# Performance work log

Hardware: AMD Instinct MI355X
Metric: run time of the kernel (lower is better)

Reference implementation:

```python
import jax, jax.numpy as jnp
import numpy as np

N_EMBD = 1024
N_HEAD = 16
HEAD_SIZE = N_EMBD // N_HEAD
EPS = 1e-5

def layer_norm(x, g, b):
    mu = jnp.mean(x, axis=-1, keepdims=True)
    var = jnp.mean(jnp.square(x - mu), axis=-1, keepdims=True)
    return (x - mu) * jax.lax.rsqrt(var + EPS) * g + b

def setup_inputs() -> dict:
    key = jax.random.key(0)
    ks = jax.random.split(key, 12)
    B, T, C, H, D = 2, 2048, N_EMBD, N_HEAD, HEAD_SIZE
    s = C ** -0.5
    return {
        "x":  jax.random.normal(ks[0], (B, T, C), jnp.float32),
        "Wq": jax.random.normal(ks[1], (H, C, D), jnp.float32) * s,
        "Wk": jax.random.normal(ks[2], (H, C, D), jnp.float32) * s,
        "Wv": jax.random.normal(ks[3], (H, C, D), jnp.float32) * s,
        "Wo": jax.random.normal(ks[4], (C, C), jnp.float32) * s,
        "bo": jnp.zeros((C,), jnp.float32),
        "g1": jnp.ones((C,), jnp.float32),
        "b1": jnp.zeros((C,), jnp.float32),
        "g2": jnp.ones((C,), jnp.float32),
        "b2": jnp.zeros((C,), jnp.float32),
        "W1": jax.random.normal(ks[5], (C, 4 * C), jnp.float32) * s,
        "bb1": jnp.zeros((4 * C,), jnp.float32),
        "W2": jax.random.normal(ks[6], (4 * C, C), jnp.float32) * (4 * C) ** -0.5,
        "bb2": jnp.zeros((C,), jnp.float32),
    }

def reference(x, Wq, Wk, Wv, Wo, bo, g1, b1, g2, b2, W1, bb1, W2, bb2):
    B, T, C = x.shape
    h = layer_norm(x, g1, b1)
    # per-head projections (no bias), stacked over heads: [B,H,T,D]
    q = jnp.einsum('btc,hcd->bhtd', h, Wq)
    k = jnp.einsum('btc,hcd->bhtd', h, Wk)
    v = jnp.einsum('btc,hcd->bhtd', h, Wv)
    # NOTE: original scales by C**-0.5 where C = n_embd (not head_size)
    scores = jnp.einsum('bhtd,bhsd->bhts', q, k) * (C ** -0.5)
    causal = jnp.tril(jnp.ones((T, T), dtype=bool))
    scores = jnp.where(causal, scores, -jnp.inf)
    wei = jax.nn.softmax(scores, axis=-1)
    y = jnp.einsum('bhts,bhsd->bhtd', wei, v)            # [B,H,T,D]
    y = jnp.transpose(y, (0, 2, 1, 3)).reshape(B, T, C)  # concat heads
    attn_out = y @ Wo + bo
    x = x + attn_out
    h2 = layer_norm(x, g2, b2)
    mlp = jax.nn.gelu(h2 @ W1 + bb1, approximate=True) @ W2 + bb2
    return x + mlp
```

## Files before the change

### kernel.cpp

```cpp
#include <hip/hip_runtime.h>
#include <cstdint>

typedef unsigned short u16;
typedef __attribute__((ext_vector_type(8))) short bf16x8;
typedef __attribute__((ext_vector_type(4))) float f32x4;

__device__ __forceinline__ u16 f2b(float f) {
  union { float f; unsigned u; } v; v.f = f;
  return (u16)((v.u + 0x7FFFu + ((v.u >> 16) & 1u)) >> 16);
}

__device__ __forceinline__ void async_copy16(void* lds, const void* g) {
  auto* l3 = reinterpret_cast<__attribute__((address_space(3))) unsigned int*>(
      reinterpret_cast<uintptr_t>(lds));
  auto* g1 = reinterpret_cast<const __attribute__((address_space(1))) unsigned int*>(
      reinterpret_cast<uintptr_t>(g));
  __builtin_amdgcn_global_load_lds(g1, l3, 16, 0, 0);
}

template<int MODE, int TN>
__global__ void gemm_bt(const u16* __restrict__ A, const u16* __restrict__ BT,
                        int M, int N, int K,
                        const float* __restrict__ bias,
                        const float* __restrict__ resid,
                        void* __restrict__ outp, float qs)
{
  constexpr int MT = (TN == 128) ? 4 : 2;
  __shared__ __align__(16) u16 sA[2][128 * 32];
  __shared__ __align__(16) u16 sB[2][TN * 32];
  const int tid = threadIdx.x;
  const int wid = tid >> 6;
  const int lane = tid & 63;
  const int L = lane & 15;
  const int Qd = lane >> 4;
  const int waveM = (TN == 128) ? (wid >> 1) : wid;
  const int waveNoff = (TN == 128) ? (wid & 1) * 64 : 0;

  const unsigned gid = blockIdx.y * gridDim.x + blockIdx.x;
  const unsigned xcd = gid & 7u;
  const unsigned t = gid >> 3;
  const unsigned ypx = gridDim.y >> 3;
  const int bmi = xcd * ypx + t / gridDim.x;
  const int bni = t % gridDim.x;
  const int bm = bmi * 128;
  const int bn = bni * TN;

  f32x4 acc[MT][4] = {};

  const int s0 = wid * 128 + lane;
  const int r0 = s0 >> 2, g0 = (s0 & 3) ^ ((r0 >> 1) & 3);
  const int s1 = s0 + 64;
  const int r1 = s1 >> 2, g1c = (s1 & 3) ^ ((r1 >> 1) & 3);
  const u16* Ar0 = A + (size_t)(bm + r0) * K + g0 * 8;
  const u16* Ar1 = A + (size_t)(bm + r1) * K + g1c * 8;
  const int t0 = (TN == 128) ? s0 : (wid * 64 + lane);
  const int q0 = t0 >> 2, h0 = (t0 & 3) ^ ((q0 >> 1) & 3);
  const u16* Br0 = BT + (size_t)(bn + q0) * K + h0 * 8;
  const int q1 = s1 >> 2, h1 = (s1 & 3) ^ ((q1 >> 1) & 3);
  const u16* Br1 = BT + (size_t)(bn + q1) * K + h1 * 8;

  const int nk = K >> 5;
  auto stage = [&](int it, int buf) {
    const int ko = it * 32;
    async_copy16(&sA[buf][(wid * 128) * 8],      Ar0 + ko);
    async_copy16(&sA[buf][(wid * 128 + 64) * 8], Ar1 + ko);
    if constexpr (TN == 128) {
      async_copy16(&sB[buf][(wid * 128) * 8],      Br0 + ko);
      async_copy16(&sB[buf][(wid * 128 + 64) * 8], Br1 + ko);
    } else {
      async_copy16(&sB[buf][(wid * 64) * 8],       Br0 + ko);
    }
  };

  stage(0, 0);
#pragma unroll 1
  for (int it = 0; it < nk; ++it) {
    const int buf = it & 1;
    __syncthreads();
    if (it + 1 < nk) stage(it + 1, buf ^ 1);

    bf16x8 af[MT], bfr[4];
#pragma unroll
    for (int mt = 0; mt < MT; ++mt) {
      int r = waveM * (MT * 16) + mt * 16 + L;
      int slot = r * 4 + (Qd ^ ((r >> 1) & 3));
      af[mt] = *(const bf16x8*)&sA[buf][slot * 8];
    }
#pragma unroll
    for (int nt = 0; nt < 4; ++nt) {
      int r = waveNoff + nt * 16 + L;
      int slot = r * 4 + (Qd ^ ((r >> 1) & 3));
      bfr[nt] = *(const bf16x8*)&sB[buf][slot * 8];
    }
#pragma unroll
    for (int mt = 0; mt < MT; ++mt)
#pragma unroll
      for (int nt = 0; nt < 4; ++nt)
        acc[mt][nt] = __builtin_amdgcn_mfma_f32_16x16x32_bf16(af[mt], bfr[nt], acc[mt][nt], 0, 0, 0);
  }

#pragma unroll
  for (int mt = 0; mt < MT; ++mt) {
#pragma unroll
    for (int nt = 0; nt < 4; ++nt) {
#pragma unroll
      for (int i = 0; i < 4; ++i) {
        int m = bm + waveM * (MT * 16) + mt * 16 + Qd * 4 + i;
        int n = bn + waveNoff + nt * 16 + L;
        float c = acc[mt][nt][i];
        if constexpr (MODE == 0) {
          float sc = (n < 1024) ? qs : 1.0f;
          ((u16*)outp)[(size_t)m * N + n] = f2b(c * sc);
        } else if constexpr (MODE == 1) {
          ((u16*)outp)[(size_t)(n >> 11) * 2097152 + (size_t)m * 2048 + (n & 2047)] = f2b(c);
        } else if constexpr (MODE == 2) {
          size_t idx = (size_t)m * N + n;
          ((float*)outp)[idx] = resid[idx] + c + bias[n];
        } else {
          float v = c + bias[n];
          float t2 = v + 0.044715f * v * v * v;
          float gl = 0.5f * v * (1.0f + tanhf(0.7978845608028654f * t2));
          ((u16*)outp)[(size_t)m * N + n] = f2b(gl);
        }
      }
    }
  }
}

__global__ void attn_kernel(const u16* __restrict__ qk, const u16* __restrict__ vT,
                            u16* __restrict__ y)
{
  __shared__ __align__(16) u16 sK[2][64 * 64];
  __shared__ __align__(16) u16 sV[2][64 * 64];
  __shared__ __align__(16) u16 sP[4 * 16 * 72];
  const int tid = threadIdx.x, wid = tid >> 6, lane = tid & 63;
  const int L = lane & 15, Qd = lane >> 4;
  const int bh = blockIdx.y, b = bh >> 4, h = bh & 15;

  const int s0 = wid * 128 + lane;
  const int rr0 = s0 >> 3, gg0 = (s0 & 7) ^ ((rr0 >> 1) & 7);
  const int s1 = s0 + 64;
  const int rr1 = s1 >> 3, gg1 = (s1 & 7) ^ ((rr1 >> 1) & 7);

  const u16* kb0 = qk + (size_t)(b * 2048 + rr0) * 2048 + 1024 + h * 64 + gg0 * 8;
  const u16* kb1 = qk + (size_t)(b * 2048 + rr1) * 2048 + 1024 + h * 64 + gg1 * 8;
  const u16* vb0 = vT + (size_t)(bh * 64 + rr0) * 2048 + gg0 * 8;
  const u16* vb1 = vT + (size_t)(bh * 64 + rr1) * 2048 + gg1 * 8;

  auto stage = [&](int kt, int buf) {
    const size_t ko = (size_t)kt * 64 * 2048;
    async_copy16(&sK[buf][(wid * 128) * 8],      kb0 + ko);
    async_copy16(&sK[buf][(wid * 128 + 64) * 8], kb1 + ko);
    async_copy16(&sV[buf][(wid * 128) * 8],      vb0 + kt * 64);
    async_copy16(&sV[buf][(wid * 128 + 64) * 8], vb1 + kt * 64);
  };

#pragma unroll 1
  for (int phase = 0; phase < 2; ++phase) {
    const int qt = phase == 0 ? (int)blockIdx.x : 31 - (int)blockIdx.x;
    const int nkt = qt + 1;

    const int qrow = b * 2048 + qt * 64 + wid * 16 + L;
    bf16x8 aq[2];
#pragma unroll
    for (int kk = 0; kk < 2; ++kk)
      aq[kk] = *(const bf16x8*)&qk[(size_t)qrow * 2048 + h * 64 + kk * 32 + Qd * 8];

    f32x4 oacc[4] = {};
    float lrow[4] = {0.f, 0.f, 0.f, 0.f};

    __syncthreads();
    stage(0, 0);

#pragma unroll 1
    for (int kt = 0; kt < nkt; ++kt) {
      const int buf = kt & 1;
      __syncthreads();
      if (kt + 1 < nkt) stage(kt + 1, buf ^ 1);

      f32x4 sacc[4] = {};
#pragma unroll
      for (int nt = 0; nt < 4; ++nt) {
        int r = nt * 16 + L;
#pragma unroll
        for (int kk = 0; kk < 2; ++kk) {
          int slot = r * 8 + ((kk * 4 + Qd) ^ ((r >> 1) & 7));
          bf16x8 bk = *(const bf16x8*)&sK[buf][slot * 8];
          sacc[nt] = __builtin_amdgcn_mfma_f32_16x16x32_bf16(aq[kk], bk, sacc[nt], 0, 0, 0);
        }
      }
      if (kt == qt) {
#pragma unroll
        for (int nt = 0; nt < 4; ++nt)
#pragma unroll
          for (int i = 0; i < 4; ++i)
            if (nt * 16 + L > wid * 16 + Qd * 4 + i) sacc[nt][i] = -__builtin_inff();
      }
#pragma unroll
      for (int nt = 0; nt < 4; ++nt)
#pragma unroll
        for (int i = 0; i < 4; ++i) {
          float p = exp2f(sacc[nt][i]);
          lrow[i] += p;
          sP[wid * 1152 + (Qd * 4 + i) * 72 + nt * 16 + L] = f2b(p);
        }
#pragma unroll
      for (int kk = 0; kk < 2; ++kk) {
        bf16x8 ap = *(const bf16x8*)&sP[wid * 1152 + L * 72 + kk * 32 + Qd * 8];
#pragma unroll
        for (int nt = 0; nt < 4; ++nt) {
          int r = nt * 16 + L;
          int slot = r * 8 + ((kk * 4 + Qd) ^ ((r >> 1) & 7));
          bf16x8 bv = *(const bf16x8*)&sV[buf][slot * 8];
          oacc[nt] = __builtin_amdgcn_mfma_f32_16x16x32_bf16(ap, bv, oacc[nt], 0, 0, 0);
        }
      }
    }

#pragma unroll
    for (int i = 0; i < 4; ++i) {
      float l = lrow[i];
      l += __shfl_xor(l, 1);
      l += __shfl_xor(l, 2);
      l += __shfl_xor(l, 4);
      l += __shfl_xor(l, 8);
      lrow[i] = l;
    }
#pragma unroll
    for (int nt = 0; nt < 4; ++nt)
#pragma unroll
      for (int i = 0; i < 4; ++i) {
        float o = oacc[nt][i] / lrow[i];
        int t = qt * 64 + wid * 16 + Qd * 4 + i;
        y[(size_t)(b * 2048 + t) * 1024 + h * 64 + nt * 16 + L] = f2b(o);
      }
  }
}

__global__ void ln_kernel(const float* __restrict__ x, const float* __restrict__ g,
                          const float* __restrict__ b, u16* __restrict__ out)
{
  const int row = blockIdx.x, tid = threadIdx.x;
  const float4 v = ((const float4*)(x + (size_t)row * 1024))[tid];
  float s = v.x + v.y + v.z + v.w;
  float s2 = v.x * v.x + v.y * v.y + v.z * v.z + v.w * v.w;
#pragma unroll
  for (int off = 1; off < 64; off <<= 1) {
    s += __shfl_xor(s, off);
    s2 += __shfl_xor(s2, off);
  }
  __shared__ float red[8];
  const int wid = tid >> 6, lane = tid & 63;
  if (lane == 0) { red[wid] = s; red[4 + wid] = s2; }
  __syncthreads();
  float S = red[0] + red[1] + red[2] + red[3];
  float S2 = red[4] + red[5] + red[6] + red[7];
  const float mu = S * (1.f / 1024.f);
  const float var = S2 * (1.f / 1024.f) - mu * mu;
  const float rs = rsqrtf(var + 1e-5f);
  const float4 gv = ((const float4*)g)[tid];
  const float4 bv = ((const float4*)b)[tid];
  ushort4 o;
  o.x = f2b((v.x - mu) * rs * gv.x + bv.x);
  o.y = f2b((v.y - mu) * rs * gv.y + bv.y);
  o.z = f2b((v.z - mu) * rs * gv.z + bv.z);
  o.w = f2b((v.w - mu) * rs * gv.w + bv.w);
  ((ushort4*)(out + (size_t)row * 1024))[tid] = o;
}

__global__ void transpose_cvt(const float* __restrict__ src, u16* __restrict__ dst,
                              int R, int C)
{
  __shared__ float tile[32][33];
  const int tx = threadIdx.x & 31, ty = threadIdx.x >> 5;
  const size_t zoff = (size_t)blockIdx.z * R * C;
  const int r0 = blockIdx.y * 32, c0 = blockIdx.x * 32;
#pragma unroll
  for (int k = 0; k < 4; ++k)
    tile[ty + k * 8][tx] = src[zoff + (size_t)(r0 + ty + k * 8) * C + c0 + tx];
  __syncthreads();
#pragma unroll
  for (int k = 0; k < 4; ++k)
    dst[zoff + (size_t)(c0 + ty + k * 8) * R + r0 + tx] = f2b(tile[tx][ty + k * 8]);
}

extern "C" void kernel_launch(void* const* d_in, const int* in_sizes, int n_in,
                              void* d_out, int out_size, void* d_ws, size_t ws_size,
                              hipStream_t stream)
{
  const float* x   = (const float*)d_in[0];
  const float* Wq  = (const float*)d_in[1];
  const float* Wk  = (const float*)d_in[2];
  const float* Wv  = (const float*)d_in[3];
  const float* Wo  = (const float*)d_in[4];
  const float* bo  = (const float*)d_in[5];
  const float* g1  = (const float*)d_in[6];
  const float* b1  = (const float*)d_in[7];
  const float* g2  = (const float*)d_in[8];
  const float* b2  = (const float*)d_in[9];
  const float* W1  = (const float*)d_in[10];
  const float* bb1 = (const float*)d_in[11];
  const float* W2  = (const float*)d_in[12];
  const float* bb2 = (const float*)d_in[13];

  char* ws = (char*)d_ws;
  const size_t MB = 1024 * 1024;
  u16*   h_bf  = (u16*)(ws);
  u16*   qkb   = (u16*)(ws + 8  * MB);
  u16*   vT    = (u16*)(ws + 24 * MB);
  u16*   y_bf  = (u16*)(ws + 32 * MB);
  float* x2    = (float*)(ws + 40 * MB);
  u16*   h2_bf = (u16*)(ws + 56 * MB);
  u16*   hid   = (u16*)(ws + 64 * MB);
  u16*   wqkv  = (u16*)(ws + 96 * MB);
  u16*   wo_bt = (u16*)(ws + 102 * MB);
  u16*   w1_bt = (u16*)(ws + 104 * MB);
  u16*   w2_bt = (u16*)(ws + 112 * MB);

  const float QSCALE = 0.04508422f;

  transpose_cvt<<<dim3(2, 32, 16), 256, 0, stream>>>(Wq, wqkv, 1024, 64);
  transpose_cvt<<<dim3(2, 32, 16), 256, 0, stream>>>(Wk, wqkv + 1024 * 1024, 1024, 64);
  transpose_cvt<<<dim3(2, 32, 16), 256, 0, stream>>>(Wv, wqkv + 2048 * 1024, 1024, 64);
  transpose_cvt<<<dim3(32, 32, 1), 256, 0, stream>>>(Wo, wo_bt, 1024, 1024);
  transpose_cvt<<<dim3(128, 32, 1), 256, 0, stream>>>(W1, w1_bt, 1024, 4096);
  transpose_cvt<<<dim3(32, 128, 1), 256, 0, stream>>>(W2, w2_bt, 4096, 1024);

  ln_kernel<<<4096, 256, 0, stream>>>(x, g1, b1, h_bf);
  gemm_bt<0, 64><<<dim3(32, 32), 256, 0, stream>>>(h_bf, wqkv, 4096, 2048, 1024, nullptr, nullptr, qkb, QSCALE);
  gemm_bt<1, 64><<<dim3(64, 8), 256, 0, stream>>>(wqkv + 2048 * 1024, h_bf, 1024, 4096, 1024, nullptr, nullptr, vT, 1.f);
  attn_kernel<<<dim3(16, 32), 256, 0, stream>>>(qkb, vT, y_bf);
  gemm_bt<2, 64><<<dim3(16, 32), 256, 0, stream>>>(y_bf, wo_bt, 4096, 1024, 1024, bo, x, x2, 1.f);
  ln_kernel<<<4096, 256, 0, stream>>>(x2, g2, b2, h2_bf);
  gemm_bt<3, 128><<<dim3(32, 32), 256, 0, stream>>>(h2_bf, w1_bt, 4096, 4096, 1024, bb1, nullptr, hid, 1.f);
  gemm_bt<2, 64><<<dim3(16, 32), 256, 0, stream>>>(hid, w2_bt, 4096, 1024, 4096, bb2, x2, d_out, 1.f);
}
```

Before: 357.6 us.

## Double GEMM K-tile to 64 and fuse weight transposes into one launch

```diff
diff --git a/kernel.cpp b/kernel.cpp
--- a/kernel.cpp
+++ b/kernel.cpp
@@ -26,8 +26,9 @@
                         void* __restrict__ outp, float qs)
 {
   constexpr int MT = (TN == 128) ? 4 : 2;
-  __shared__ __align__(16) u16 sA[2][128 * 32];
-  __shared__ __align__(16) u16 sB[2][TN * 32];
+  constexpr int BCALLS = TN / 32;
+  __shared__ __align__(16) u16 sA[2][128 * 64];
+  __shared__ __align__(16) u16 sB[2][TN * 64];
   const int tid = threadIdx.x;
   const int wid = tid >> 6;
   const int lane = tid & 63;
@@ -47,29 +48,30 @@
 
   f32x4 acc[MT][4] = {};
 
-  const int s0 = wid * 128 + lane;
-  const int r0 = s0 >> 2, g0 = (s0 & 3) ^ ((r0 >> 1) & 3);
-  const int s1 = s0 + 64;
-  const int r1 = s1 >> 2, g1c = (s1 & 3) ^ ((r1 >> 1) & 3);
-  const u16* Ar0 = A + (size_t)(bm + r0) * K + g0 * 8;
-  const u16* Ar1 = A + (size_t)(bm + r1) * K + g1c * 8;
-  const int t0 = (TN == 128) ? s0 : (wid * 64 + lane);
-  const int q0 = t0 >> 2, h0 = (t0 & 3) ^ ((q0 >> 1) & 3);
-  const u16* Br0 = BT + (size_t)(bn + q0) * K + h0 * 8;
-  const int q1 = s1 >> 2, h1 = (s1 & 3) ^ ((q1 >> 1) & 3);
-  const u16* Br1 = BT + (size_t)(bn + q1) * K + h1 * 8;
-
-  const int nk = K >> 5;
+  const u16* Asrc[4];
+#pragma unroll
+  for (int j = 0; j < 4; ++j) {
+    int s = wid * 256 + j * 64 + lane;
+    int r = s >> 3, c = (s & 7) ^ (r & 7);
+    Asrc[j] = A + (size_t)(bm + r) * K + c * 8;
+  }
+  const u16* Bsrc[BCALLS];
+#pragma unroll
+  for (int j = 0; j < BCALLS; ++j) {
+    int s = wid * (BCALLS * 64) + j * 64 + lane;
+    int r = s >> 3, c = (s & 7) ^ (r & 7);
+    Bsrc[j] = BT + (size_t)(bn + r) * K + c * 8;
+  }
+
+  const int nk = K >> 6;
   auto stage = [&](int it, int buf) {
-    const int ko = it * 32;
-    async_copy16(&sA[buf][(wid * 128) * 8],      Ar0 + ko);
-    async_copy16(&sA[buf][(wid * 128 + 64) * 8], Ar1 + ko);
-    if constexpr (TN == 128) {
-      async_copy16(&sB[buf][(wid * 128) * 8],      Br0 + ko);
-      async_copy16(&sB[buf][(wid * 128 + 64) * 8], Br1 + ko);
-    } else {
-      async_copy16(&sB[buf][(wid * 64) * 8],       Br0 + ko);
-    }
+    const int ko = it * 64;
+#pragma unroll
+    for (int j = 0; j < 4; ++j)
+      async_copy16(&sA[buf][(wid * 256 + j * 64) * 8], Asrc[j] + ko);
+#pragma unroll
+    for (int j = 0; j < BCALLS; ++j)
+      async_copy16(&sB[buf][(wid * (BCALLS * 64) + j * 64) * 8], Bsrc[j] + ko);
   };
 
   stage(0, 0);
@@ -79,24 +81,32 @@
     __syncthreads();
     if (it + 1 < nk) stage(it + 1, buf ^ 1);
 
-    bf16x8 af[MT], bfr[4];
+    bf16x8 af[MT][2], bfr[4][2];
 #pragma unroll
     for (int mt = 0; mt < MT; ++mt) {
       int r = waveM * (MT * 16) + mt * 16 + L;
-      int slot = r * 4 + (Qd ^ ((r >> 1) & 3));
-      af[mt] = *(const bf16x8*)&sA[buf][slot * 8];
+#pragma unroll
+      for (int kk = 0; kk < 2; ++kk) {
+        int slot = r * 8 + ((kk * 4 + Qd) ^ (r & 7));
+        af[mt][kk] = *(const bf16x8*)&sA[buf][slot * 8];
+      }
     }
 #pragma unroll
     for (int nt = 0; nt < 4; ++nt) {
       int r = waveNoff + nt * 16 + L;
-      int slot = r * 4 + (Qd ^ ((r >> 1) & 3));
-      bfr[nt] = *(const bf16x8*)&sB[buf][slot * 8];
-    }
-#pragma unroll
-    for (int mt = 0; mt < MT; ++mt)
-#pragma unroll
-      for (int nt = 0; nt < 4; ++nt)
-        acc[mt][nt] = __builtin_amdgcn_mfma_f32_16x16x32_bf16(af[mt], bfr[nt], acc[mt][nt], 0, 0, 0);
+#pragma unroll
+      for (int kk = 0; kk < 2; ++kk) {
+        int slot = r * 8 + ((kk * 4 + Qd) ^ (r & 7));
+        bfr[nt][kk] = *(const bf16x8*)&sB[buf][slot * 8];
+      }
+    }
+#pragma unroll
+    for (int kk = 0; kk < 2; ++kk)
+#pragma unroll
+      for (int mt = 0; mt < MT; ++mt)
+#pragma unroll
+        for (int nt = 0; nt < 4; ++nt)
+          acc[mt][nt] = __builtin_amdgcn_mfma_f32_16x16x32_bf16(af[mt][kk], bfr[nt][kk], acc[mt][nt], 0, 0, 0);
   }
 
 #pragma unroll
@@ -268,13 +278,35 @@
   ((ushort4*)(out + (size_t)row * 1024))[tid] = o;
 }
 
-__global__ void transpose_cvt(const float* __restrict__ src, u16* __restrict__ dst,
-                              int R, int C)
+__global__ void transpose_all(const float* __restrict__ Wq, const float* __restrict__ Wk,
+                              const float* __restrict__ Wv, const float* __restrict__ Wo,
+                              const float* __restrict__ W1, const float* __restrict__ W2,
+                              u16* __restrict__ wqkv, u16* __restrict__ wo_bt,
+                              u16* __restrict__ w1_bt, u16* __restrict__ w2_bt)
 {
   __shared__ float tile[32][33];
+  const int id = blockIdx.x;
+  const float* src; u16* dst; int R, C, tx32, ty32; size_t zoff = 0;
+  if (id < 3072) {
+    int m = id >> 10;
+    src = (m == 0) ? Wq : (m == 1) ? Wk : Wv;
+    dst = wqkv + (size_t)m * 1024 * 1024;
+    int r = id & 1023;
+    zoff = (size_t)(r >> 6) * 1024 * 64;
+    int t = r & 63;
+    R = 1024; C = 64; tx32 = t & 1; ty32 = t >> 1;
+  } else if (id < 4096) {
+    src = Wo; dst = wo_bt; R = 1024; C = 1024;
+    int t = id - 3072; tx32 = t & 31; ty32 = t >> 5;
+  } else if (id < 8192) {
+    src = W1; dst = w1_bt; R = 1024; C = 4096;
+    int t = id - 4096; tx32 = t & 127; ty32 = t >> 7;
+  } else {
+    src = W2; dst = w2_bt; R = 4096; C = 1024;
+    int t = id - 8192; tx32 = t & 31; ty32 = t >> 5;
+  }
   const int tx = threadIdx.x & 31, ty = threadIdx.x >> 5;
-  const size_t zoff = (size_t)blockIdx.z * R * C;
-  const int r0 = blockIdx.y * 32, c0 = blockIdx.x * 32;
+  const int r0 = ty32 * 32, c0 = tx32 * 32;
 #pragma unroll
   for (int k = 0; k < 4; ++k)
     tile[ty + k * 8][tx] = src[zoff + (size_t)(r0 + ty + k * 8) * C + c0 + tx];
@@ -319,12 +351,8 @@
 
   const float QSCALE = 0.04508422f;
 
-  transpose_cvt<<<dim3(2, 32, 16), 256, 0, stream>>>(Wq, wqkv, 1024, 64);
-  transpose_cvt<<<dim3(2, 32, 16), 256, 0, stream>>>(Wk, wqkv + 1024 * 1024, 1024, 64);
-  transpose_cvt<<<dim3(2, 32, 16), 256, 0, stream>>>(Wv, wqkv + 2048 * 1024, 1024, 64);
-  transpose_cvt<<<dim3(32, 32, 1), 256, 0, stream>>>(Wo, wo_bt, 1024, 1024);
-  transpose_cvt<<<dim3(128, 32, 1), 256, 0, stream>>>(W1, w1_bt, 1024, 4096);
-  transpose_cvt<<<dim3(32, 128, 1), 256, 0, stream>>>(W2, w2_bt, 4096, 1024);
+  transpose_all<<<12288, 256, 0, stream>>>(Wq, Wk, Wv, Wo, W1, W2,
+                                           wqkv, wo_bt, w1_bt, w2_bt);
 
   ln_kernel<<<4096, 256, 0, stream>>>(x, g1, b1, h_bf);
   gemm_bt<0, 64><<<dim3(32, 32), 256, 0, stream>>>(h_bf, wqkv, 4096, 2048, 1024, nullptr, nullptr, qkb, QSCALE);
```

Result: faster. 335.9 us (-6.1%).
